# Kernel tuning notes

Measured on AMD Instinct MI355X. Metric: run time of the kernel, lower is better.

The kernel has to match this reference:

```python
import jax, jax.numpy as jnp
import numpy as np

STEPS = 4
EMB = 128
HEADS = 3
NUM_GRAPHS = 64
NODES_PER = 64
N = NUM_GRAPHS * NODES_PER
E_SPARSE = N * 16
DATA_LENS = [NODES_PER] * NUM_GRAPHS


def _complete_edge_index(data_lens):
    # dense_to_sparse(complete_matrix) -> all (i,j) pairs within each block,
    # including self loops (diagonal of complete_matrix is 1).
    srcs, dsts = [], []
    start = 0
    for l in data_lens:
        idx = np.arange(start, start + l)
        srcs.append(np.repeat(idx, l))
        dsts.append(np.tile(idx, l))
        start += l
    return np.stack([np.concatenate(srcs), np.concatenate(dsts)]).astype(np.int32)


def leaky(x, slope=0.01):
    return jnp.where(x >= 0, x, slope * x)


def setup_inputs() -> dict:
    key = jax.random.key(0)
    ks = jax.random.split(key, 16)
    s = 0.05
    edge_complete = jnp.asarray(_complete_edge_index(DATA_LENS))
    # sparse edge_index: random edges within each graph
    src_local = jax.random.randint(ks[1], (E_SPARSE,), 0, NODES_PER)
    dst_local = jax.random.randint(ks[2], (E_SPARSE,), 0, NODES_PER)
    gid = jnp.repeat(jnp.arange(NUM_GRAPHS), E_SPARSE // NUM_GRAPHS) * NODES_PER
    edge_index = jnp.stack([src_local + gid, dst_local + gid]).astype(jnp.int32)
    batch_ind = jnp.repeat(jnp.arange(NUM_GRAPHS), NODES_PER).astype(jnp.int32)
    return {
        "x": jax.random.normal(ks[0], (N, EMB), jnp.float32),
        "edge_index": edge_index,
        "batch_ind": batch_ind,
        "edge_complete": edge_complete,
        "Wm": jax.random.normal(ks[3], (STEPS, EMB, EMB)) * s,
        "bm": jnp.zeros((STEPS, EMB)),
        "Wa": jax.random.normal(ks[4], (STEPS, 3 * EMB, EMB)) * s,
        "ba": jnp.zeros((STEPS, EMB)),
        "Wl": jax.random.normal(ks[5], (STEPS - 1, EMB, HEADS * EMB)) * s,
        "bl": jnp.zeros((STEPS - 1, HEADS * EMB)),
        "Wr": jax.random.normal(ks[6], (STEPS - 1, EMB, HEADS * EMB)) * s,
        "br": jnp.zeros((STEPS - 1, HEADS * EMB)),
        "att_w": jax.random.normal(ks[7], (STEPS - 1, HEADS, EMB)) * s,
        "att_bias": jnp.zeros((STEPS - 1, EMB)),
    }


def _graphnet(x, x_att, batch_ind, src, dst, Wm, bm, Wa, ba):
    # message: f_mess(x_j)  (edge_attr is None in this model)
    m = leaky(x[src] @ Wm + bm)                               # [E, D]
    agg = jax.ops.segment_max(m, dst, num_segments=x.shape[0])
    agg = jnp.where(jnp.isneginf(agg), 0.0, agg)              # PyG fills empty with 0
    xg = x_att[batch_ind]                                     # [N, D]
    z = jnp.concatenate([x, xg, agg], axis=1)                 # [N, 3D]
    return leaky(z @ Wa + ba) + x


def _gatv2(x, src, dst, Wl, bl, Wr, br, att, bias):
    n = x.shape[0]
    xl = (x @ Wl + bl).reshape(n, HEADS, EMB)                 # source transform
    xr = (x @ Wr + br).reshape(n, HEADS, EMB)                 # target transform
    e = leaky(xl[src] + xr[dst], 0.2)                         # [E, H, D]
    logits = jnp.einsum('ehd,hd->eh', e, att)                 # [E, H]
    mx = jax.ops.segment_max(logits, dst, num_segments=n)
    mx = jnp.where(jnp.isneginf(mx), 0.0, mx)
    alpha = jnp.exp(logits - mx[dst])
    denom = jax.ops.segment_sum(alpha, dst, num_segments=n)
    alpha = alpha / denom[dst]                                # softmax over incoming edges
    out = jax.ops.segment_sum(alpha[:, :, None] * xl[src], dst, num_segments=n)
    return out.mean(axis=1) + bias                            # concat=False -> head mean


def reference(x, edge_index, batch_ind, edge_complete, Wm, bm, Wa, ba, Wl, bl, Wr, br, att_w, att_bias):
    src, dst = edge_index[0], edge_index[1]
    csrc, cdst = edge_complete[0], edge_complete[1]
    x_att = jnp.zeros((NUM_GRAPHS, EMB), x.dtype)
    for i in range(STEPS):
        x = _graphnet(x, x_att, batch_ind, src, dst, Wm[i], bm[i], Wa[i], ba[i])
        if i < STEPS - 1:
            x_att_nodes = leaky(_gatv2(x, csrc, cdst, Wl[i], bl[i], Wr[i], br[i], att_w[i], att_bias[i]))
            # original indexes xg = x_att[batch_ind]; x_att here is per-node, so
            # emulate torch semantics: x_att has len(x) rows, indexed by batch_ind.
            x_att = x_att_nodes
        # note: in original, x_att has shape [len(x), emb]; xg = x_att[batch_ind]
    return x


if __name__ == "__main__":
    out = reference(**setup_inputs())
    print(out.shape)
```

## Files before the change

kernel.cpp:

```cpp
#include <hip/hip_runtime.h>
#include <math.h>

#define D 128
#define GB 64
#define BT 1024
#define ZP 264
#define XLP 74

typedef __attribute__((ext_vector_type(8))) short bf16x8;
typedef __attribute__((ext_vector_type(4))) float f32x4;
typedef __attribute__((ext_vector_type(4))) unsigned u32x4;

__device__ __forceinline__ float leaky01(float v) { return v >= 0.f ? v : 0.01f * v; }
__device__ __forceinline__ unsigned short f2bf(float f) {
    unsigned u = __float_as_uint(f);
    u += 0x7FFFu + ((u >> 16) & 1u);
    return (unsigned short)(u >> 16);
}
__device__ __forceinline__ float bf2f(unsigned short s) {
    return __uint_as_float(((unsigned)s) << 16);
}

__device__ __forceinline__ void st_sys_u32(unsigned* p, unsigned v) {
    asm volatile("global_store_dword %0, %1, off sc0 sc1" :: "v"(p), "v"(v) : "memory");
}
__device__ __forceinline__ void st_sys_u128(unsigned* p, u32x4 v) {
    asm volatile("global_store_dwordx4 %0, %1, off sc0 sc1" :: "v"(p), "v"(v) : "memory");
}
__device__ __forceinline__ unsigned ld_sys_u32(const unsigned* p) {
    unsigned v;
    asm volatile("global_load_dword %0, %1, off sc0 sc1\n\ts_waitcnt vmcnt(0)"
                 : "=v"(v) : "v"(p) : "memory");
    return v;
}
__device__ __forceinline__ u32x4 ld_sys_u128(const unsigned* p) {
    u32x4 v;
    asm volatile("global_load_dwordx4 %0, %1, off sc0 sc1\n\ts_waitcnt vmcnt(0)"
                 : "=v"(v) : "v"(p) : "memory");
    return v;
}
__device__ __forceinline__ void waitst() { asm volatile("s_waitcnt vmcnt(0)" ::: "memory"); }

__global__ void k_wconv(const float* __restrict__ Wm, const float* __restrict__ Wa,
                        const float* __restrict__ Wl,
                        unsigned short* __restrict__ Wmt, unsigned short* __restrict__ Wat,
                        unsigned short* __restrict__ Wlt,
                        unsigned* __restrict__ flags) {
    int gid = blockIdx.x * blockDim.x + threadIdx.x;
    if (blockIdx.x == 0 && threadIdx.x < 8) st_sys_u32(&flags[threadIdx.x], 0u);
    if (gid < 16384) {
        int o = gid * 4;
        int s = o >> 14, rem = o & 16383, n = rem >> 7, k0 = rem & 127;
        const float* src = Wm + (size_t)s * 16384;
        unsigned short* dst = Wmt + o;
#pragma unroll
        for (int j = 0; j < 4; ++j) dst[j] = f2bf(src[(size_t)(k0 + j) * 128 + n]);
    } else if (gid < 49152) {
        int o = (gid - 16384) * 4;
        int s = o >> 15, rem = o & 32767, n = rem >> 8, k0 = rem & 255;
        int row = (k0 < 128) ? k0 : (k0 + 128);
        const float* src = Wa + (size_t)s * 49152;
        unsigned short* dst = Wat + o;
#pragma unroll
        for (int j = 0; j < 4; ++j) dst[j] = f2bf(src[(size_t)(row + j) * 128 + n]);
    } else if (gid < 86016) {
        int o = (gid - 49152) * 4;
        int s = o / 49152, rem = o % 49152, n = rem >> 7, k0 = rem & 127;
        const float* src = Wl + (size_t)s * 49152;
        unsigned short* dst = Wlt + o;
#pragma unroll
        for (int j = 0; j < 4; ++j) dst[j] = f2bf(src[(size_t)(k0 + j) * 384 + n]);
    }
}

struct Args {
    const float* x0;
    const int* e_src; const int* e_dst;
    const unsigned short *Wmt, *Wat, *Wlt;
    const float *Wa, *Wr, *bm, *ba, *bl, *br, *att_w, *att_bias;
    unsigned short* xg0;
    unsigned* flagX;
    float* out;
};

__global__ __launch_bounds__(BT) void k_mega(Args p) {
    const int tid = threadIdx.x, bid = blockIdx.x, g = bid;
    const int wave = tid >> 6, lane = tid & 63;
    const int m16 = lane & 15, kg = lane >> 4;
    const int wtile = wave >> 1;
    const int half = wave & 1;
    const int col = wtile * 16 + m16;

    __shared__ unsigned short zsb[64][ZP];
    __shared__ unsigned short hs[64][128];
    __shared__ unsigned short xl3[3][128][XLP];
    __shared__ float red[3072];
    __shared__ unsigned mlo[64], mhi[64];
    __shared__ float att_s[3][D];
    __shared__ float xgrow[D];
    __shared__ float ygmid[D];
    __shared__ float xr3[384];
    __shared__ float alpha3[192];

    unsigned short (*xg_s)[128] = (unsigned short(*)[128])&hs[0][0];

    if (tid < 64) { mlo[tid] = 0u; mhi[tid] = 0u; }
    __syncthreads();
    {
        int i0 = g * 1024 + tid;
        int s1 = p.e_src[i0] - g * 64, d1 = p.e_dst[i0] - g * 64;
        atomicOr(s1 < 32 ? &mlo[d1] : &mhi[d1], 1u << (s1 & 31));
    }

    float xreg[8];
    {
        const float* xp = p.x0 + (size_t)g * 64 * D;
#pragma unroll
        for (int i = 0; i < 2; ++i) {
            int mt = half * 2 + i;
#pragma unroll
            for (int r = 0; r < 4; ++r)
                xreg[i * 4 + r] = xp[(mt * 16 + kg * 4 + r) * D + col];
        }
    }
    __syncthreads();

    for (int step = 0; step < 4; ++step) {
#pragma unroll
        for (int i = 0; i < 2; ++i) {
            int mt = half * 2 + i;
#pragma unroll
            for (int r = 0; r < 4; ++r) zsb[mt * 16 + kg * 4 + r][col] = f2bf(xreg[i * 4 + r]);
        }
        if (step < 3 && tid < 384) att_s[tid >> 7][tid & 127] = p.att_w[step * 384 + tid];
        __syncthreads();

        {
            const unsigned short* Wb = p.Wmt + ((size_t)(step * 128 + col) * 128 + kg * 8);
            bf16x8 bB[4];
#pragma unroll
            for (int kt = 0; kt < 4; ++kt) bB[kt] = *(const bf16x8*)(Wb + kt * 32);
            float bb = p.bm[step * 128 + col];
#pragma unroll
            for (int i = 0; i < 2; ++i) {
                int mt = half * 2 + i;
                f32x4 acc = {0.f, 0.f, 0.f, 0.f};
#pragma unroll
                for (int kt = 0; kt < 4; ++kt) {
                    bf16x8 a = *(const bf16x8*)&zsb[mt * 16 + m16][kt * 32 + kg * 8];
                    acc = __builtin_amdgcn_mfma_f32_16x16x32_bf16(a, bB[kt], acc, 0, 0, 0);
                }
#pragma unroll
                for (int r = 0; r < 4; ++r)
                    hs[mt * 16 + kg * 4 + r][col] = f2bf(leaky01(acc[r] + bb));
            }
        }
        __syncthreads();

        {
            int r0 = wave * 4;
            unsigned lo[4], hi[4];
#pragma unroll
            for (int r = 0; r < 4; ++r) {
                lo[r] = (unsigned)__builtin_amdgcn_readfirstlane((int)mlo[r0 + r]);
                hi[r] = (unsigned)__builtin_amdgcn_readfirstlane((int)mhi[r0 + r]);
            }
            float m0[4], m1[4];
#pragma unroll
            for (int r = 0; r < 4; ++r) { m0[r] = -INFINITY; m1[r] = -INFINITY; }
#pragma unroll 4
            for (int s = 0; s < 32; ++s) {
                unsigned hv = *(const unsigned*)&hs[s][lane * 2];
                float v0 = bf2f((unsigned short)(hv & 0xffffu));
                float v1 = bf2f((unsigned short)(hv >> 16));
#pragma unroll
                for (int r = 0; r < 4; ++r)
                    if ((lo[r] >> s) & 1u) { m0[r] = fmaxf(m0[r], v0); m1[r] = fmaxf(m1[r], v1); }
            }
#pragma unroll 4
            for (int s = 32; s < 64; ++s) {
                unsigned hv = *(const unsigned*)&hs[s][lane * 2];
                float v0 = bf2f((unsigned short)(hv & 0xffffu));
                float v1 = bf2f((unsigned short)(hv >> 16));
#pragma unroll
                for (int r = 0; r < 4; ++r)
                    if ((hi[r] >> (s - 32)) & 1u) { m0[r] = fmaxf(m0[r], v0); m1[r] = fmaxf(m1[r], v1); }
            }
#pragma unroll
            for (int r = 0; r < 4; ++r) {
                unsigned pk = (lo[r] | hi[r])
                                  ? (((unsigned)f2bf(m1[r]) << 16) | (unsigned)f2bf(m0[r]))
                                  : 0u;
                *(unsigned*)&zsb[r0 + r][128 + lane * 2] = pk;
            }
        }

        if (step > 0) {
            int n = tid & 127, q = tid >> 7;
            float a = 0.f;
            const float* Wmid = p.Wa + (size_t)step * 49152 + (size_t)(128 + q * 16) * 128 + n;
#pragma unroll 8
            for (int k2 = 0; k2 < 16; ++k2) a += xgrow[q * 16 + k2] * Wmid[(size_t)k2 * 128];
            red[q * 128 + n] = a;
            __syncthreads();
            if (tid < 128) {
                float s8 = 0.f;
#pragma unroll
                for (int q2 = 0; q2 < 8; ++q2) s8 += red[q2 * 128 + tid];
                ygmid[tid] = s8;
            }
        }
        __syncthreads();

        {
            const unsigned short* Wb = p.Wat + ((size_t)(step * 128 + col) * 256 + kg * 8);
            bf16x8 bB[8];
#pragma unroll
            for (int kt = 0; kt < 8; ++kt) bB[kt] = *(const bf16x8*)(Wb + kt * 32);
            float extra = p.ba[step * 128 + col] + (step > 0 ? ygmid[col] : 0.f);
#pragma unroll
            for (int i = 0; i < 2; ++i) {
                int mt = half * 2 + i;
                f32x4 acc = {0.f, 0.f, 0.f, 0.f};
#pragma unroll
                for (int kt = 0; kt < 8; ++kt) {
                    bf16x8 a = *(const bf16x8*)&zsb[mt * 16 + m16][kt * 32 + kg * 8];
                    acc = __builtin_amdgcn_mfma_f32_16x16x32_bf16(a, bB[kt], acc, 0, 0, 0);
                }
#pragma unroll
                for (int r = 0; r < 4; ++r) {
                    float v = leaky01(acc[r] + extra) + xreg[i * 4 + r];
                    xreg[i * 4 + r] = v;
                    if (step == 3) p.out[((size_t)g * 64 + mt * 16 + kg * 4 + r) * D + col] = v;
                }
            }
        }

        if (step < 3) {
            __syncthreads();
            unsigned short* xg0g = p.xg0 + (size_t)step * 8192;
            if (bid == 0) {
#pragma unroll
                for (int i = 0; i < 2; ++i) {
                    int mt = half * 2 + i;
#pragma unroll
                    for (int r = 0; r < 4; ++r) {
                        int row = mt * 16 + kg * 4 + r;
                        unsigned off = (unsigned)(row * 256 + col * 2) ^ (unsigned)((row & 7) << 4);
                        *(unsigned short*)((char*)&xg_s[0][0] + off) = f2bf(xreg[i * 4 + r]);
                    }
                }
                __syncthreads();
                {
                    unsigned boff = (unsigned)tid * 16;
                    int row = tid >> 4;
                    u32x4 v = *(u32x4*)((char*)&xg_s[0][0] + (boff ^ (unsigned)((row & 7) << 4)));
                    st_sys_u128((unsigned*)((char*)xg0g + boff), v);
                }
                waitst();
                __syncthreads();
                if (tid == 0) st_sys_u32(p.flagX + step, 1u);
            } else {
                if (tid == 0) {
                    int it = 0;
                    while (ld_sys_u32(p.flagX + step) == 0 && it++ < (1 << 22))
                        __builtin_amdgcn_s_sleep(2);
                }
                __syncthreads();
                {
                    unsigned boff = (unsigned)tid * 16;
                    int row = tid >> 4;
                    u32x4 v = ld_sys_u128((const unsigned*)((const char*)xg0g + boff));
                    *(u32x4*)((char*)&xg_s[0][0] + (boff ^ (unsigned)((row & 7) << 4))) = v;
                }
                __syncthreads();
            }

            for (int h = 0; h < 3; ++h) {
                const unsigned short* Wb = p.Wlt + ((size_t)(step * 384 + h * 128 + col) * 128 + kg * 8);
                bf16x8 bB[4];
#pragma unroll
                for (int kt = 0; kt < 4; ++kt) bB[kt] = *(const bf16x8*)(Wb + kt * 32);
                float bb = p.bl[step * 384 + h * 128 + col];
#pragma unroll
                for (int i = 0; i < 2; ++i) {
                    int mt = half * 2 + i;
                    f32x4 acc = {0.f, 0.f, 0.f, 0.f};
#pragma unroll
                    for (int kt = 0; kt < 4; ++kt) {
                        int row = mt * 16 + m16;
                        unsigned off = (unsigned)(row * 256 + (kt * 32 + kg * 8) * 2) ^ (unsigned)((row & 7) << 4);
                        bf16x8 a = *(const bf16x8*)((const char*)&xg_s[0][0] + off);
                        acc = __builtin_amdgcn_mfma_f32_16x16x32_bf16(a, bB[kt], acc, 0, 0, 0);
                    }
                    int s0 = mt * 16 + kg * 4;
                    unsigned pk0 = (unsigned)f2bf(acc[0] + bb) | ((unsigned)f2bf(acc[1] + bb) << 16);
                    unsigned pk1 = (unsigned)f2bf(acc[2] + bb) | ((unsigned)f2bf(acc[3] + bb) << 16);
                    *(unsigned*)&xl3[h][col][s0] = pk0;
                    *(unsigned*)&xl3[h][col][s0 + 2] = pk1;
                }
            }
            if (tid < 768) {
                int q = (tid >= 384) ? 1 : 0;
                int n3 = tid - q * 384;
                int h = n3 >> 7, n = n3 & 127;
                float a = 0.f;
                const float* Wrp = p.Wr + (size_t)step * 49152 + (size_t)(q * 64) * 384 + h * 128 + n;
#pragma unroll 8
                for (int k2 = 0; k2 < 64; ++k2) {
                    int k = q * 64 + k2;
                    unsigned b = ((unsigned)(g * 256 + k * 2)) ^ (unsigned)((g & 7) << 4);
                    float xv = bf2f(*(const unsigned short*)((const char*)&xg_s[0][0] + b));
                    a += xv * Wrp[(size_t)k2 * 384];
                }
                red[q * 384 + n3] = a;
            }
            __syncthreads();
            if (tid < 384) xr3[tid] = red[tid] + red[384 + tid] + p.br[step * 384 + tid];
            __syncthreads();

            {
                int kb = wave * 8;
#pragma unroll
                for (int h = 0; h < 3; ++h) {
                    float part = 0.f;
#pragma unroll
                    for (int kk = 0; kk < 8; ++kk) {
                        int k = kb + kk;
                        float t = bf2f(xl3[h][k][lane]) + xr3[h * 128 + k];
                        t = (t >= 0.f) ? t : 0.2f * t;
                        part += att_s[h][k] * t;
                    }
                    red[(h * 16 + wave) * 64 + lane] = part;
                }
            }
            __syncthreads();
            if (tid < 192) {
                int h = tid >> 6;
                float lg = 0.f;
#pragma unroll
                for (int w2 = 0; w2 < 16; ++w2) lg += red[(h * 16 + w2) * 64 + lane];
                float mx = lg;
#pragma unroll
                for (int o = 32; o > 0; o >>= 1) mx = fmaxf(mx, __shfl_xor(mx, o));
                float a = __expf(lg - mx), sm = a;
#pragma unroll
                for (int o = 32; o > 0; o >>= 1) sm += __shfl_xor(sm, o);
                alpha3[h * 64 + lane] = a / sm;
            }
            __syncthreads();

            {
                int c = tid & 127, q = tid >> 7;
                if (q < 6) {
                    int h = q >> 1, sq = q & 1;
                    float pv = 0.f;
#pragma unroll
                    for (int s2 = 0; s2 < 32; ++s2) {
                        int s = sq * 32 + s2;
                        pv += alpha3[h * 64 + s] * bf2f(xl3[h][c][s]);
                    }
                    red[q * 128 + c] = pv;
                }
            }
            __syncthreads();
            if (tid < 128) {
                float accO = red[tid] + red[128 + tid] + red[256 + tid]
                           + red[384 + tid] + red[512 + tid] + red[640 + tid];
                xgrow[tid] = leaky01(accO * (1.f / 3.f) + p.att_bias[step * 128 + tid]);
            }
        }
        __syncthreads();
    }
}

extern "C" void kernel_launch(void* const* d_in, const int* in_sizes, int n_in,
                              void* d_out, int out_size, void* d_ws, size_t ws_size,
                              hipStream_t stream) {
    (void)n_in; (void)out_size; (void)ws_size;
    const float* x_in     = (const float*)d_in[0];
    const int*   edge_idx = (const int*)d_in[1];
    const float* Wm  = (const float*)d_in[4];
    const float* bm  = (const float*)d_in[5];
    const float* Wa  = (const float*)d_in[6];
    const float* ba  = (const float*)d_in[7];
    const float* Wl  = (const float*)d_in[8];
    const float* bl  = (const float*)d_in[9];
    const float* Wr  = (const float*)d_in[10];
    const float* br  = (const float*)d_in[11];
    const float* att_w    = (const float*)d_in[12];
    const float* att_bias = (const float*)d_in[13];
    const int E = in_sizes[1] / 2;

    char* ws = (char*)d_ws;
    size_t off = 0;
    auto alloc = [&](size_t bytes) { void* pp = ws + off; off += (bytes + 255) & ~size_t(255); return pp; };
    unsigned short* xg0 = (unsigned short*)alloc((size_t)3 * 64 * 128 * 2);
    unsigned short* Wmt = (unsigned short*)alloc((size_t)4 * 128 * 128 * 2);
    unsigned short* Wat = (unsigned short*)alloc((size_t)4 * 128 * 256 * 2);
    unsigned short* Wlt = (unsigned short*)alloc((size_t)3 * 384 * 128 * 2);
    unsigned* flags     = (unsigned*)alloc(8 * 4);

    k_wconv<<<336, 256, 0, stream>>>(Wm, Wa, Wl, Wmt, Wat, Wlt, flags);

    Args a;
    a.x0 = x_in;
    a.e_src = edge_idx;
    a.e_dst = edge_idx + E;
    a.Wmt = Wmt; a.Wat = Wat; a.Wlt = Wlt;
    a.Wa = Wa; a.Wr = Wr; a.bm = bm; a.ba = ba; a.bl = bl; a.br = br;
    a.att_w = att_w; a.att_bias = att_bias;
    a.xg0 = xg0; a.flagX = flags;
    a.out = (float*)d_out;
    void* kargs[] = { (void*)&a };
    (void)hipLaunchCooperativeKernel((void*)k_mega, dim3(GB), dim3(BT), kargs, 0, stream);
}
```

Measured before the change: 147.1 us.

## Cut block barriers by deferring reductions and computing softmax in-wave

Removes several __syncthreads by folding small reductions (ygmid, xr3, xgrow) into their consumers, using separate regions of an enlarged shared scratch buffer, and deferring the xgrow finalisation to the start of the next step. The softmax alpha is now computed redundantly in each consuming wave and broadcast with shuffles instead of going through shared memory. The neighbour max aggregation iterates only over set adjacency bits with ctz instead of scanning all 64 sources. The Wa weight fragment loads are hoisted earlier to overlap with the aggregation. The trade-off is some duplicated arithmetic and more shared memory.

```diff
diff --git a/kernel.cpp b/kernel.cpp
--- a/kernel.cpp
+++ b/kernel.cpp
@@ -94,13 +94,11 @@
     __shared__ unsigned short zsb[64][ZP];
     __shared__ unsigned short hs[64][128];
     __shared__ unsigned short xl3[3][128][XLP];
-    __shared__ float red[3072];
+    __shared__ float red[4608];
     __shared__ unsigned mlo[64], mhi[64];
     __shared__ float att_s[3][D];
+    __shared__ float br_s[384];
     __shared__ float xgrow[D];
-    __shared__ float ygmid[D];
-    __shared__ float xr3[384];
-    __shared__ float alpha3[192];
 
     unsigned short (*xg_s)[128] = (unsigned short(*)[128])&hs[0][0];
 
@@ -126,13 +124,21 @@
     __syncthreads();
 
     for (int step = 0; step < 4; ++step) {
+        if (step > 0 && tid < 128) {
+            float accO = red[3840 + tid] + red[3840 + 128 + tid] + red[3840 + 256 + tid]
+                       + red[3840 + 384 + tid] + red[3840 + 512 + tid] + red[3840 + 640 + tid];
+            xgrow[tid] = leaky01(accO * (1.f / 3.f) + p.att_bias[(step - 1) * 128 + tid]);
+        }
 #pragma unroll
         for (int i = 0; i < 2; ++i) {
             int mt = half * 2 + i;
 #pragma unroll
             for (int r = 0; r < 4; ++r) zsb[mt * 16 + kg * 4 + r][col] = f2bf(xreg[i * 4 + r]);
         }
-        if (step < 3 && tid < 384) att_s[tid >> 7][tid & 127] = p.att_w[step * 384 + tid];
+        if (step < 3 && tid < 384) {
+            att_s[tid >> 7][tid & 127] = p.att_w[step * 384 + tid];
+            br_s[tid] = p.br[step * 384 + tid];
+        }
         __syncthreads();
 
         {
@@ -157,44 +163,12 @@
         }
         __syncthreads();
 
+        bf16x8 wat[8];
         {
-            int r0 = wave * 4;
-            unsigned lo[4], hi[4];
-#pragma unroll
-            for (int r = 0; r < 4; ++r) {
-                lo[r] = (unsigned)__builtin_amdgcn_readfirstlane((int)mlo[r0 + r]);
-                hi[r] = (unsigned)__builtin_amdgcn_readfirstlane((int)mhi[r0 + r]);
-            }
-            float m0[4], m1[4];
-#pragma unroll
-            for (int r = 0; r < 4; ++r) { m0[r] = -INFINITY; m1[r] = -INFINITY; }
-#pragma unroll 4
-            for (int s = 0; s < 32; ++s) {
-                unsigned hv = *(const unsigned*)&hs[s][lane * 2];
-                float v0 = bf2f((unsigned short)(hv & 0xffffu));
-                float v1 = bf2f((unsigned short)(hv >> 16));
-#pragma unroll
-                for (int r = 0; r < 4; ++r)
-                    if ((lo[r] >> s) & 1u) { m0[r] = fmaxf(m0[r], v0); m1[r] = fmaxf(m1[r], v1); }
-            }
-#pragma unroll 4
-            for (int s = 32; s < 64; ++s) {
-                unsigned hv = *(const unsigned*)&hs[s][lane * 2];
-                float v0 = bf2f((unsigned short)(hv & 0xffffu));
-                float v1 = bf2f((unsigned short)(hv >> 16));
-#pragma unroll
-                for (int r = 0; r < 4; ++r)
-                    if ((hi[r] >> (s - 32)) & 1u) { m0[r] = fmaxf(m0[r], v0); m1[r] = fmaxf(m1[r], v1); }
-            }
-#pragma unroll
-            for (int r = 0; r < 4; ++r) {
-                unsigned pk = (lo[r] | hi[r])
-                                  ? (((unsigned)f2bf(m1[r]) << 16) | (unsigned)f2bf(m0[r]))
-                                  : 0u;
-                *(unsigned*)&zsb[r0 + r][128 + lane * 2] = pk;
-            }
-        }
-
+            const unsigned short* WbU = p.Wat + ((size_t)(step * 128 + col) * 256 + kg * 8);
+#pragma unroll
+            for (int kt = 0; kt < 8; ++kt) wat[kt] = *(const bf16x8*)(WbU + kt * 32);
+        }
         if (step > 0) {
             int n = tid & 127, q = tid >> 7;
             float a = 0.f;
@@ -202,22 +176,37 @@
 #pragma unroll 8
             for (int k2 = 0; k2 < 16; ++k2) a += xgrow[q * 16 + k2] * Wmid[(size_t)k2 * 128];
             red[q * 128 + n] = a;
-            __syncthreads();
-            if (tid < 128) {
-                float s8 = 0.f;
-#pragma unroll
-                for (int q2 = 0; q2 < 8; ++q2) s8 += red[q2 * 128 + tid];
-                ygmid[tid] = s8;
+        }
+        {
+            int r0 = wave * 4;
+#pragma unroll
+            for (int r = 0; r < 4; ++r) {
+                int row = r0 + r;
+                unsigned lo = (unsigned)__builtin_amdgcn_readfirstlane((int)mlo[row]);
+                unsigned hi = (unsigned)__builtin_amdgcn_readfirstlane((int)mhi[row]);
+                unsigned long long mk = (((unsigned long long)hi) << 32) | lo;
+                float m0 = -INFINITY, m1 = -INFINITY;
+                unsigned long long t = mk;
+                while (t) {
+                    int s = __builtin_ctzll(t);
+                    t &= t - 1;
+                    unsigned hv = *(const unsigned*)&hs[s][lane * 2];
+                    m0 = fmaxf(m0, bf2f((unsigned short)(hv & 0xffffu)));
+                    m1 = fmaxf(m1, bf2f((unsigned short)(hv >> 16)));
+                }
+                unsigned pk = mk ? (((unsigned)f2bf(m1) << 16) | (unsigned)f2bf(m0)) : 0u;
+                *(unsigned*)&zsb[row][128 + lane * 2] = pk;
             }
         }
         __syncthreads();
 
         {
-            const unsigned short* Wb = p.Wat + ((size_t)(step * 128 + col) * 256 + kg * 8);
-            bf16x8 bB[8];
-#pragma unroll
-            for (int kt = 0; kt < 8; ++kt) bB[kt] = *(const bf16x8*)(Wb + kt * 32);
-            float extra = p.ba[step * 128 + col] + (step > 0 ? ygmid[col] : 0.f);
+            float yg = 0.f;
+            if (step > 0) {
+#pragma unroll
+                for (int q2 = 0; q2 < 8; ++q2) yg += red[q2 * 128 + col];
+            }
+            float extra = p.ba[step * 128 + col] + yg;
 #pragma unroll
             for (int i = 0; i < 2; ++i) {
                 int mt = half * 2 + i;
@@ -225,7 +214,7 @@
 #pragma unroll
                 for (int kt = 0; kt < 8; ++kt) {
                     bf16x8 a = *(const bf16x8*)&zsb[mt * 16 + m16][kt * 32 + kg * 8];
-                    acc = __builtin_amdgcn_mfma_f32_16x16x32_bf16(a, bB[kt], acc, 0, 0, 0);
+                    acc = __builtin_amdgcn_mfma_f32_16x16x32_bf16(a, wat[kt], acc, 0, 0, 0);
                 }
 #pragma unroll
                 for (int r = 0; r < 4; ++r) {
@@ -234,12 +223,7 @@
                     if (step == 3) p.out[((size_t)g * 64 + mt * 16 + kg * 4 + r) * D + col] = v;
                 }
             }
-        }
-
-        if (step < 3) {
-            __syncthreads();
-            unsigned short* xg0g = p.xg0 + (size_t)step * 8192;
-            if (bid == 0) {
+            if (bid == 0 && step < 3) {
 #pragma unroll
                 for (int i = 0; i < 2; ++i) {
                     int mt = half * 2 + i;
@@ -250,7 +234,13 @@
                         *(unsigned short*)((char*)&xg_s[0][0] + off) = f2bf(xreg[i * 4 + r]);
                     }
                 }
-                __syncthreads();
+            }
+        }
+        __syncthreads();
+
+        if (step < 3) {
+            unsigned short* xg0g = p.xg0 + (size_t)step * 8192;
+            if (bid == 0) {
                 {
                     unsigned boff = (unsigned)tid * 16;
                     int row = tid >> 4;
@@ -260,6 +250,7 @@
                 waitst();
                 __syncthreads();
                 if (tid == 0) st_sys_u32(p.flagX + step, 1u);
+                __syncthreads();
             } else {
                 if (tid == 0) {
                     int it = 0;
@@ -313,10 +304,8 @@
                     float xv = bf2f(*(const unsigned short*)((const char*)&xg_s[0][0] + b));
                     a += xv * Wrp[(size_t)k2 * 384];
                 }
-                red[q * 384 + n3] = a;
-            }
-            __syncthreads();
-            if (tid < 384) xr3[tid] = red[tid] + red[384 + tid] + p.br[step * 384 + tid];
+                red[3072 + q * 384 + n3] = a;
+            }
             __syncthreads();
 
             {
@@ -327,7 +316,9 @@
 #pragma unroll
                     for (int kk = 0; kk < 8; ++kk) {
                         int k = kb + kk;
-                        float t = bf2f(xl3[h][k][lane]) + xr3[h * 128 + k];
+                        float xr = red[3072 + h * 128 + k] + red[3072 + 384 + h * 128 + k]
+                                 + br_s[h * 128 + k];
+                        float t = bf2f(xl3[h][k][lane]) + xr;
                         t = (t >= 0.f) ? t : 0.2f * t;
                         part += att_s[h][k] * t;
                     }
@@ -335,42 +326,33 @@
                 }
             }
             __syncthreads();
-            if (tid < 192) {
-                int h = tid >> 6;
-                float lg = 0.f;
-#pragma unroll
-                for (int w2 = 0; w2 < 16; ++w2) lg += red[(h * 16 + w2) * 64 + lane];
-                float mx = lg;
-#pragma unroll
-                for (int o = 32; o > 0; o >>= 1) mx = fmaxf(mx, __shfl_xor(mx, o));
-                float a = __expf(lg - mx), sm = a;
-#pragma unroll
-                for (int o = 32; o > 0; o >>= 1) sm += __shfl_xor(sm, o);
-                alpha3[h * 64 + lane] = a / sm;
-            }
-            __syncthreads();
 
             {
-                int c = tid & 127, q = tid >> 7;
+                int q = tid >> 7, c = tid & 127;
                 if (q < 6) {
                     int h = q >> 1, sq = q & 1;
+                    float lg = 0.f;
+#pragma unroll
+                    for (int w2 = 0; w2 < 16; ++w2) lg += red[(h * 16 + w2) * 64 + lane];
+                    float mx = lg;
+#pragma unroll
+                    for (int o = 32; o > 0; o >>= 1) mx = fmaxf(mx, __shfl_xor(mx, o));
+                    float a = __expf(lg - mx), sm = a;
+#pragma unroll
+                    for (int o = 32; o > 0; o >>= 1) sm += __shfl_xor(sm, o);
+                    float alpha = a / sm;
                     float pv = 0.f;
 #pragma unroll
                     for (int s2 = 0; s2 < 32; ++s2) {
                         int s = sq * 32 + s2;
-                        pv += alpha3[h * 64 + s] * bf2f(xl3[h][c][s]);
+                        float as = __shfl(alpha, s);
+                        pv += as * bf2f(xl3[h][c][s]);
                     }
-                    red[q * 128 + c] = pv;
+                    red[3840 + q * 128 + c] = pv;
                 }
             }
             __syncthreads();
-            if (tid < 128) {
-                float accO = red[tid] + red[128 + tid] + red[256 + tid]
-                           + red[384 + tid] + red[512 + tid] + red[640 + tid];
-                xgrow[tid] = leaky01(accO * (1.f / 3.f) + p.att_bias[step * 128 + tid]);
-            }
-        }
-        __syncthreads();
+        }
     }
 }
 
```

Measured after the change: 123.0 us. 16.4% less time.
